# Kernel tuning notes

Measured on AMD Instinct MI355X. Metric: run time of the kernel, lower is better.

The kernel has to match this reference:

```python
import jax, jax.numpy as jnp
import numpy as np

B, N, S, D, K = 8, 8192, 2048, 256, 3
MLP = [256, 128]
EPS = 1e-5


def setup_inputs() -> dict:
    key = jax.random.key(0)
    ks = jax.random.split(key, 12)
    inp = {
        "xyz1": jax.random.normal(ks[0], (B, N, 3), dtype=jnp.float32),
        "xyz2": jax.random.normal(ks[1], (B, S, 3), dtype=jnp.float32),
        "points1": jax.random.normal(ks[2], (B, N, D), dtype=jnp.float32),
        "points2": jax.random.normal(ks[3], (B, S, D), dtype=jnp.float32),
        # relation conv: Conv2d(4 -> 1, kernel 1x1) == linear over last dim
        "rel_w": jax.random.normal(ks[4], (4,), dtype=jnp.float32) * 0.5,
        "rel_b": jnp.zeros((), dtype=jnp.float32),
        # mlp layer 0: Conv1d(2D -> 256, k=1) + BN
        "W0": jax.random.normal(ks[5], (MLP[0], 2 * D), dtype=jnp.float32) * (1.0 / np.sqrt(2 * D)),
        "b0": jnp.zeros((MLP[0],), dtype=jnp.float32),
        "g0": jnp.ones((MLP[0],), dtype=jnp.float32),
        "be0": jnp.zeros((MLP[0],), dtype=jnp.float32),
        # mlp layer 1: Conv1d(256 -> 128, k=1) + BN
        "W1": jax.random.normal(ks[6], (MLP[1], MLP[0]), dtype=jnp.float32) * (1.0 / np.sqrt(MLP[0])),
        "b1": jnp.zeros((MLP[1],), dtype=jnp.float32),
        "g1": jnp.ones((MLP[1],), dtype=jnp.float32),
        "be1": jnp.zeros((MLP[1],), dtype=jnp.float32),
    }
    return inp


def _gather(points, idx):
    # points: [B,S,C], idx: [B,N,K] -> [B,N,K,C]
    return jax.vmap(lambda p, i: p[i])(points, idx)


def _bn_relu(x, gamma, beta):
    # training-mode BatchNorm1d over [B,N,C]: stats over (B,N), biased var
    mean = jnp.mean(x, axis=(0, 1))
    var = jnp.var(x, axis=(0, 1))
    xn = (x - mean) * jax.lax.rsqrt(var + EPS)
    return jax.nn.relu(xn * gamma + beta)


def reference(xyz1, xyz2, points1, points2, rel_w, rel_b,
              W0, b0, g0, be0, W1, b1, g1, be1):
    # pairwise squared distances [B,N,S]
    d = (jnp.sum(xyz1 ** 2, -1)[:, :, None]
         + jnp.sum(xyz2 ** 2, -1)[:, None, :]
         - 2.0 * jnp.einsum('bnc,bmc->bnm', xyz1, xyz2))
    neg_d, idx = jax.lax.top_k(-d, K)          # K smallest distances
    dists = -neg_d                              # [B,N,K]

    offset = xyz1[:, :, None, :] - _gather(xyz2, idx)        # [B,N,K,3]
    rel = jnp.concatenate([dists[..., None], offset], -1)    # [B,N,K,4]
    weight = jax.nn.sigmoid(rel @ rel_w + rel_b)              # [B,N,K]

    interp = jnp.mean(_gather(points2, idx) * weight[..., None], axis=2)  # [B,N,D]
    h = jnp.concatenate([points1, interp], axis=-1)           # [B,N,2D]

    h = _bn_relu(jnp.einsum('bnc,oc->bno', h, W0) + b0, g0, be0)
    h = _bn_relu(jnp.einsum('bnc,oc->bno', h, W1) + b1, g1, be1)
    return h  # [B,N,128]
```

## Files before the change

kernel.cpp:

```cpp
#include <hip/hip_runtime.h>
#include <stdint.h>
#include <stddef.h>

#define B_   8
#define N_   8192
#define S_   2048
#define D_   256
#define M_   (B_*N_)
#define C0_  256
#define C1_  128
#define K2D_ 512
#define TS8_ 8
#define SEG8_ (S_/TS8_)
#define SWP_ 264

typedef __attribute__((ext_vector_type(8))) short short8;
typedef __attribute__((ext_vector_type(4))) float f32x4;
typedef __attribute__((ext_vector_type(2))) float f32x2;

__device__ __forceinline__ short f2bf(float f) {
  unsigned u = __float_as_uint(f);
  u += 0x7fffu + ((u >> 16) & 1u);
  return (short)(u >> 16);
}
__device__ __forceinline__ float bf2f(short s) {
  return __uint_as_float(((unsigned)(unsigned short)s) << 16);
}

__device__ __forceinline__ void cp16(const void* g, void* l) {
  __builtin_amdgcn_global_load_lds(
      (__attribute__((address_space(1))) void*)(g),
      (__attribute__((address_space(3))) void*)(l), 16, 0, 0);
}

#define INS3(v, si)                                                           \
  {                                                                           \
    const float v_ = (v); const int s_ = (si);                                \
    const bool b0 = v_ < d0, b1 = v_ < d1, b2 = v_ < d2;                      \
    const int   ni2 = b1 ? i1 : (b2 ? s_ : i2);                               \
    const float nd2 = __builtin_amdgcn_fmed3f(v_, d1, d2);                    \
    const int   ni1 = b0 ? i0 : (b1 ? s_ : i1);                               \
    const float nd1 = __builtin_amdgcn_fmed3f(v_, d0, d1);                    \
    const int   ni0 = b0 ? s_ : i0;                                           \
    const float nd0 = fminf(v_, d0);                                          \
    d0 = nd0; d1 = nd1; d2 = nd2; i0 = ni0; i1 = ni1; i2 = ni2;               \
  }

__global__ void convw_kernel(const float* __restrict__ W0,
                             const float* __restrict__ W1,
                             const float* __restrict__ xyz2,
                             short* __restrict__ W0b, short* __restrict__ W1b,
                             float* __restrict__ xyz2p, float* __restrict__ stats) {
  int i = blockIdx.x * 256 + threadIdx.x;
  if (blockIdx.x == 0) {
    stats[threadIdx.x] = 0.f;
    stats[256 + threadIdx.x] = 0.f;
    stats[512 + threadIdx.x] = 0.f;
  }
  if (i < C0_ * K2D_) W0b[i] = f2bf(W0[i]);
  if (i < C1_ * C0_)  W1b[i] = f2bf(W1[i]);
  if (i < B_ * S_) {
    const int b = i >> 11, s = i & (S_ - 1);
    float x = xyz2[(size_t)i * 3 + 0];
    float y = xyz2[(size_t)i * 3 + 1];
    float z = xyz2[(size_t)i * 3 + 2];
    float ss = __fadd_rn(__fadd_rn(__fmul_rn(x, x), __fmul_rn(y, y)), __fmul_rn(z, z));
    float* xw = xyz2p + (size_t)b * 4 * S_;
    xw[s] = x; xw[S_ + s] = y; xw[2 * S_ + s] = z; xw[3 * S_ + s] = ss;
  }
}

__global__ __launch_bounds__(512, 8)
void topk_interp_kernel(const float* __restrict__ xyz1, const float* __restrict__ xyz2p,
                        const float* __restrict__ relw, const float* __restrict__ relb,
                        const float* __restrict__ p2, short* __restrict__ hi) {
  __shared__ float cd[TS8_][64][3];
  __shared__ int   ci[TS8_][64][3];
  __shared__ int   sj[64][3];
  __shared__ float sw[64][3];
  const int tid  = threadIdx.x;
  const int lane = tid & 63;
  const int seg  = __builtin_amdgcn_readfirstlane(tid >> 6);
  const int b    = blockIdx.x >> 7;
  const int n    = (blockIdx.x & 127) * 64 + lane;

  const float* p = xyz1 + ((size_t)b * N_ + n) * 3;
  const float ax = p[0], ay = p[1], az = p[2];
  const float s1 = __fadd_rn(__fadd_rn(__fmul_rn(ax, ax), __fmul_rn(ay, ay)), __fmul_rn(az, az));

  const float* xw = xyz2p + (size_t)b * 4 * S_;
  const f32x2* XP = (const f32x2*)(xw)           + seg * (SEG8_ / 2);
  const f32x2* YP = (const f32x2*)(xw + S_)      + seg * (SEG8_ / 2);
  const f32x2* ZP = (const f32x2*)(xw + 2 * S_)  + seg * (SEG8_ / 2);
  const f32x2* WP = (const f32x2*)(xw + 3 * S_)  + seg * (SEG8_ / 2);

  float d0 = 3.4e38f, d1 = 3.4e38f, d2 = 3.4e38f;
  int   i0 = 0, i1 = 0, i2 = 0;
  const int sbeg = seg * SEG8_;
  {
    #pragma clang fp contract(off)
    #pragma unroll 4
    for (int pr = 0; pr < SEG8_ / 2; pr++) {
      f32x2 X = XP[pr], Y = YP[pr], Z = ZP[pr], W = WP[pr];
      f32x2 t1 = ax * X;
      f32x2 t2 = ay * Y;
      f32x2 t3 = az * Z;
      f32x2 dt = (t1 + t2) + t3;
      f32x2 e  = s1 + W;
      f32x2 m  = 2.0f * dt;
      f32x2 d  = e - m;
      const float dlo = d.x, dhi = d.y;
      const int s = sbeg + 2 * pr;
      INS3(dlo, s);
      INS3(dhi, s + 1);
    }
  }
  cd[seg][lane][0] = d0; cd[seg][lane][1] = d1; cd[seg][lane][2] = d2;
  ci[seg][lane][0] = i0; ci[seg][lane][1] = i1; ci[seg][lane][2] = i2;
  __syncthreads();

  if (tid < 64) {
    float d0 = 3.4e38f, d1 = 3.4e38f, d2 = 3.4e38f;
    int   i0 = 0, i1 = 0, i2 = 0;
    #pragma unroll
    for (int sg = 0; sg < TS8_; sg++) {
      #pragma unroll
      for (int k = 0; k < 3; k++) {
        const float dv = cd[sg][tid][k];
        const int   iv = ci[sg][tid][k];
        INS3(dv, iv);
      }
    }
    const float w0r = relw[0], w1r = relw[1], w2r = relw[2], w3r = relw[3], br = relb[0];
    float dd[3] = {d0, d1, d2};
    int   ii[3] = {i0, i1, i2};
    #pragma unroll
    for (int k = 0; k < 3; k++) {
      const int s = ii[k];
      float ox = ax - xw[s], oy = ay - xw[S_ + s], oz = az - xw[2 * S_ + s];
      float t = dd[k] * w0r + ox * w1r + oy * w2r + oz * w3r + br;
      float w = 1.0f / (1.0f + expf(-t));
      sj[tid][k] = s;
      sw[tid][k] = w * (1.0f / 3.0f);
    }
  }
  __syncthreads();

  {
    const int r = tid >> 3;
    const int c0 = (tid & 7) * 32;
    const size_t rowg = (size_t)b * N_ + (size_t)(blockIdx.x & 127) * 64 + r;
    const int j0 = sj[r][0], j1 = sj[r][1], j2 = sj[r][2];
    const float w0 = sw[r][0], w1 = sw[r][1], w2 = sw[r][2];
    const float* pb = p2 + (size_t)b * S_ * D_ + c0;
    const float* q0 = pb + (size_t)j0 * D_;
    const float* q1 = pb + (size_t)j1 * D_;
    const float* q2 = pb + (size_t)j2 * D_;
    short* dst = hi + rowg * D_ + c0;
    #pragma unroll
    for (int cc = 0; cc < 32; cc += 8) {
      const float4 a0 = *(const float4*)(q0 + cc), e0 = *(const float4*)(q0 + cc + 4);
      const float4 a1 = *(const float4*)(q1 + cc), e1 = *(const float4*)(q1 + cc + 4);
      const float4 a2 = *(const float4*)(q2 + cc), e2 = *(const float4*)(q2 + cc + 4);
      float fv[8];
      fv[0] = w0 * a0.x + w1 * a1.x + w2 * a2.x;
      fv[1] = w0 * a0.y + w1 * a1.y + w2 * a2.y;
      fv[2] = w0 * a0.z + w1 * a1.z + w2 * a2.z;
      fv[3] = w0 * a0.w + w1 * a1.w + w2 * a2.w;
      fv[4] = w0 * e0.x + w1 * e1.x + w2 * e2.x;
      fv[5] = w0 * e0.y + w1 * e1.y + w2 * e2.y;
      fv[6] = w0 * e0.z + w1 * e1.z + w2 * e2.z;
      fv[7] = w0 * e0.w + w1 * e1.w + w2 * e2.w;
      short8 o;
      #pragma unroll
      for (int e = 0; e < 8; e++) o[e] = f2bf(fv[e]);
      *(short8*)(dst + cc) = o;
    }
  }
}

__global__ __launch_bounds__(256, 2)
void gemm1_kernel(const float* __restrict__ p1, const short* __restrict__ hi,
                  const short* __restrict__ Bw, const float* __restrict__ bias,
                  short* __restrict__ Cb, float* __restrict__ stats) {
  __shared__ __align__(16) short sA[2][128 * 32];
  __shared__ __align__(16) short sB[2][256 * 32];
  const int tid = threadIdx.x;
  const int lane = tid & 63;
  const int wave = tid >> 6;
  const int wm = wave & 1;
  const int wn = wave >> 1;
  const size_t mbase = (size_t)(blockIdx.x & 7) * N_
                     + (size_t)(blockIdx.x >> 3) * 128;

  #define STAGE_A(K0, BUF)                                                    \
    if ((K0) < D_) {                                                          \
      _Pragma("unroll")                                                       \
      for (int t = 0; t < 2; t++) {                                           \
        const int c = tid * 2 + t;                                            \
        const int r = c >> 2; const int sc = (c & 3) * 8;                     \
        const float* src = p1 + (mbase + r) * D_ + (K0) + sc;                 \
        const float4 va = *(const float4*)src;                                \
        const float4 vb = *(const float4*)(src + 4);                          \
        short8 o;                                                             \
        o[0] = f2bf(va.x); o[1] = f2bf(va.y); o[2] = f2bf(va.z);              \
        o[3] = f2bf(va.w); o[4] = f2bf(vb.x); o[5] = f2bf(vb.y);              \
        o[6] = f2bf(vb.z); o[7] = f2bf(vb.w);                                 \
        *(short8*)&sA[BUF][r * 32 + sc] = o;                                  \
      }                                                                       \
    } else {                                                                  \
      _Pragma("unroll")                                                       \
      for (int t = 0; t < 2; t++) {                                           \
        const int ca = wave * 128 + t * 64 + lane;                            \
        cp16(hi + (mbase + (ca >> 2)) * D_ + ((K0) - D_) + (ca & 3) * 8,      \
             &sA[BUF][(wave * 128 + t * 64) * 8]);                            \
      }                                                                       \
    }

  #define STAGE_B(K0, BUF)                                                    \
    _Pragma("unroll")                                                         \
    for (int t = 0; t < 4; t++) {                                             \
      const int cb = wave * 256 + t * 64 + lane;                              \
      cp16(Bw + (size_t)(cb >> 2) * K2D_ + (K0) + (cb & 3) * 8,               \
           &sB[BUF][(wave * 256 + t * 64) * 8]);                              \
    }

  f32x4 acc[4][8] = {};
  STAGE_A(0, 0);
  STAGE_B(0, 0);

  const int mr = lane & 15;
  const int ks = (lane >> 4) * 8;

  for (int k0 = 0, it = 0; k0 < K2D_; k0 += 32, it++) {
    __syncthreads();
    const int kn = k0 + 32;
    if (kn < K2D_) {
      STAGE_A(kn, (it + 1) & 1);
      STAGE_B(kn, (it + 1) & 1);
    }

    short8 af[4], bfr[8];
    #pragma unroll
    for (int i = 0; i < 4; i++)
      af[i]  = *(const short8*)&sA[it & 1][(wm * 64 + i * 16 + mr) * 32 + ks];
    #pragma unroll
    for (int j = 0; j < 8; j++)
      bfr[j] = *(const short8*)&sB[it & 1][(wn * 128 + j * 16 + mr) * 32 + ks];
    #pragma unroll
    for (int i = 0; i < 4; i++)
      #pragma unroll
      for (int j = 0; j < 8; j++)
        acc[i][j] = __builtin_amdgcn_mfma_f32_16x16x32_bf16(af[i], bfr[j], acc[i][j], 0, 0, 0);
  }
  #undef STAGE_A
  #undef STAGE_B
  __syncthreads();

  const int cr = (lane >> 4) * 4;
  const int cc = lane & 15;
  float ps[8], ps2[8];
  #pragma unroll
  for (int j = 0; j < 8; j++) {
    const int col = wn * 128 + j * 16 + cc;
    const float bv = bias[col];
    float s = 0.f, s2 = 0.f;
    #pragma unroll
    for (int i = 0; i < 4; i++) {
      #pragma unroll
      for (int r = 0; r < 4; r++) {
        const float vv = acc[i][j][r];
        s += vv; s2 += vv * vv;
        const size_t row = mbase + wm * 64 + i * 16 + cr + r;
        Cb[row * C0_ + col] = f2bf(vv + bv);
      }
    }
    ps[j] = s; ps2[j] = s2;
  }
  #pragma unroll
  for (int j = 0; j < 8; j++) {
    ps[j]  += __shfl_xor(ps[j], 16);  ps[j]  += __shfl_xor(ps[j], 32);
    ps2[j] += __shfl_xor(ps2[j], 16); ps2[j] += __shfl_xor(ps2[j], 32);
  }
  float* sred = (float*)sA;
  if (wm == 1 && lane < 16) {
    #pragma unroll
    for (int j = 0; j < 8; j++) {
      const int c = wn * 128 + j * 16 + lane;
      sred[2 * c] = ps[j]; sred[2 * c + 1] = ps2[j];
    }
  }
  __syncthreads();
  if (wm == 0 && lane < 16) {
    #pragma unroll
    for (int j = 0; j < 8; j++) {
      const int c = wn * 128 + j * 16 + lane;
      atomicAdd(&stats[c],       ps[j]  + sred[2 * c]);
      atomicAdd(&stats[C0_ + c], ps2[j] + sred[2 * c + 1]);
    }
  }
}

__global__ __launch_bounds__(256, 2)
void gemm2_kernel(const short* __restrict__ A, const short* __restrict__ Bw,
                  const float* __restrict__ ssn, const float* __restrict__ bias,
                  short* __restrict__ Cb, float* __restrict__ stats) {
  __shared__ __align__(16) short sW[C1_ * SWP_];
  __shared__ float sred[3 * 256];
  const int tid = threadIdx.x;
  const int lane = tid & 63;
  const int wave = tid >> 6;
  const size_t mbase = (size_t)blockIdx.x * 128;

  #pragma unroll
  for (int i = 0; i < 16; i++) {
    const int flat = i * 256 + tid;
    const int n = flat >> 5;
    const int kb = flat & 31;
    *(short8*)&sW[n * SWP_ + kb * 8] = *(const short8*)(Bw + (size_t)flat * 8);
  }
  __syncthreads();

  f32x4 acc[2][8] = {};
  const int mr = lane & 15;
  const int ksq = (lane >> 4) * 8;

  for (int k0 = 0; k0 < C0_; k0 += 32) {
    const int kk = k0 + ksq;
    float4 sc0 = *(const float4*)(ssn + kk);
    float4 sc1 = *(const float4*)(ssn + kk + 4);
    float4 sh0 = *(const float4*)(ssn + C0_ + kk);
    float4 sh1 = *(const float4*)(ssn + C0_ + kk + 4);
    const float sc[8] = {sc0.x, sc0.y, sc0.z, sc0.w, sc1.x, sc1.y, sc1.z, sc1.w};
    const float sh[8] = {sh0.x, sh0.y, sh0.z, sh0.w, sh1.x, sh1.y, sh1.z, sh1.w};
    short8 af[2];
    #pragma unroll
    for (int i = 0; i < 2; i++) {
      const size_t row = mbase + wave * 32 + i * 16 + mr;
      short8 av = *(const short8*)(A + row * C0_ + kk);
      short8 o;
      #pragma unroll
      for (int e = 0; e < 8; e++) {
        float f = bf2f(av[e]) * sc[e] + sh[e];
        o[e] = f2bf(f > 0.f ? f : 0.f);
      }
      af[i] = o;
    }
    short8 bf8[8];
    #pragma unroll
    for (int j = 0; j < 8; j++) bf8[j] = *(const short8*)&sW[(j * 16 + mr) * SWP_ + kk];
    #pragma unroll
    for (int i = 0; i < 2; i++)
      #pragma unroll
      for (int j = 0; j < 8; j++)
        acc[i][j] = __builtin_amdgcn_mfma_f32_16x16x32_bf16(af[i], bf8[j], acc[i][j], 0, 0, 0);
  }

  const int cr = (lane >> 4) * 4;
  const int cc = lane & 15;
  float ps[8], ps2[8];
  #pragma unroll
  for (int j = 0; j < 8; j++) {
    const int col = j * 16 + cc;
    const float bv = bias[col];
    float s = 0.f, s2 = 0.f;
    #pragma unroll
    for (int i = 0; i < 2; i++) {
      #pragma unroll
      for (int r = 0; r < 4; r++) {
        const float vv = acc[i][j][r];
        s += vv; s2 += vv * vv;
        const size_t row = mbase + wave * 32 + i * 16 + cr + r;
        Cb[row * C1_ + col] = f2bf(vv + bv);
      }
    }
    ps[j] = s; ps2[j] = s2;
  }
  #pragma unroll
  for (int j = 0; j < 8; j++) {
    ps[j]  += __shfl_xor(ps[j], 16);  ps[j]  += __shfl_xor(ps[j], 32);
    ps2[j] += __shfl_xor(ps2[j], 16); ps2[j] += __shfl_xor(ps2[j], 32);
  }
  if (wave > 0 && lane < 16) {
    #pragma unroll
    for (int j = 0; j < 8; j++) {
      const int c = j * 16 + lane;
      sred[(wave - 1) * 256 + c]       = ps[j];
      sred[(wave - 1) * 256 + 128 + c] = ps2[j];
    }
  }
  __syncthreads();
  if (wave == 0 && lane < 16) {
    #pragma unroll
    for (int j = 0; j < 8; j++) {
      const int c = j * 16 + lane;
      float s  = ps[j]  + sred[c]       + sred[256 + c]       + sred[512 + c];
      float s2 = ps2[j] + sred[128 + c] + sred[256 + 128 + c] + sred[512 + 128 + c];
      atomicAdd(&stats[c],       s);
      atomicAdd(&stats[C1_ + c], s2);
    }
  }
}

__global__ void stats_final_kernel(const float* __restrict__ stats, const int C,
                                   const float* __restrict__ bias,
                                   const float* __restrict__ g, const float* __restrict__ be,
                                   float* __restrict__ ss) {
  const int c = threadIdx.x;
  if (c >= C) return;
  const float inv = 1.0f / (float)M_;
  float m0 = stats[c] * inv;
  float var = stats[C + c] * inv - m0 * m0;
  float mean = m0 + bias[c];
  float sc = g[c] * rsqrtf(var + 1e-5f);
  ss[c] = sc;
  ss[C + c] = be[c] - mean * sc;
}

__global__ __launch_bounds__(256, 1)
void norm2_kernel(const short* __restrict__ a2, const float* __restrict__ ss,
                  float* __restrict__ out) {
  const size_t t = (size_t)blockIdx.x * 256 + threadIdx.x;
  const size_t base = t * 8;
  const int c = (int)(base & (C1_ - 1));
  short8 v8 = *(const short8*)(a2 + base);
  float vv[8];
  #pragma unroll
  for (int k = 0; k < 8; k++) {
    float v = bf2f(v8[k]) * ss[c + k] + ss[C1_ + c + k];
    vv[k] = v > 0.f ? v : 0.f;
  }
  *(float4*)(out + base)     = make_float4(vv[0], vv[1], vv[2], vv[3]);
  *(float4*)(out + base + 4) = make_float4(vv[4], vv[5], vv[6], vv[7]);
}

extern "C" void kernel_launch(void* const* d_in, const int* in_sizes, int n_in,
                              void* d_out, int out_size, void* d_ws, size_t ws_size,
                              hipStream_t stream) {
  const float* xyz1 = (const float*)d_in[0];
  const float* xyz2 = (const float*)d_in[1];
  const float* pts1 = (const float*)d_in[2];
  const float* pts2 = (const float*)d_in[3];
  const float* relw = (const float*)d_in[4];
  const float* relb = (const float*)d_in[5];
  const float* W0   = (const float*)d_in[6];
  const float* b0   = (const float*)d_in[7];
  const float* g0   = (const float*)d_in[8];
  const float* be0  = (const float*)d_in[9];
  const float* W1   = (const float*)d_in[10];
  const float* b1   = (const float*)d_in[11];
  const float* g1   = (const float*)d_in[12];
  const float* be1  = (const float*)d_in[13];

  char* ws = (char*)d_ws;
  constexpr size_t W0B_OFF = 0;
  constexpr size_t W1B_OFF = W0B_OFF + (size_t)C0_ * K2D_ * 2;
  constexpr size_t XW_OFF  = W1B_OFF + (size_t)C1_ * C0_ * 2;
  constexpr size_t HI_OFF  = XW_OFF + (size_t)B_ * 4 * S_ * 4;
  constexpr size_t A1_OFF  = HI_OFF + (size_t)M_ * D_ * 2;
  constexpr size_t A2_OFF  = A1_OFF + (size_t)M_ * C0_ * 2;
  constexpr size_t ST_OFF  = A2_OFF + (size_t)M_ * C1_ * 2;
  constexpr size_t SS1_OFF = ST_OFF + (size_t)768 * 4;
  constexpr size_t SS2_OFF = SS1_OFF + (size_t)2 * C0_ * 4;

  short* W0b   = (short*)(ws + W0B_OFF);
  short* W1b   = (short*)(ws + W1B_OFF);
  float* xyz2p = (float*)(ws + XW_OFF);
  short* hi    = (short*)(ws + HI_OFF);
  short* a1    = (short*)(ws + A1_OFF);
  short* a2    = (short*)(ws + A2_OFF);
  float* st    = (float*)(ws + ST_OFF);
  float* ss1   = (float*)(ws + SS1_OFF);
  float* ss2   = (float*)(ws + SS2_OFF);
  float* outp  = (float*)d_out;

  convw_kernel<<<512, 256, 0, stream>>>(W0, W1, xyz2, W0b, W1b, xyz2p, st);
  topk_interp_kernel<<<B_ * (N_ / 64), 512, 0, stream>>>(xyz1, xyz2p, relw, relb, pts2, hi);

  gemm1_kernel<<<M_ / 128, 256, 0, stream>>>(pts1, hi, W0b, b0, a1, st);
  stats_final_kernel<<<1, 256, 0, stream>>>(st, C0_, b0, g0, be0, ss1);

  gemm2_kernel<<<M_ / 128, 256, 0, stream>>>(a1, W1b, ss1, b1, a2, st + 512);
  stats_final_kernel<<<1, 128, 0, stream>>>(st + 512, C1_, b1, g1, be1, ss2);
  norm2_kernel<<<(size_t)M_ * C1_ / 8 / 256, 256, 0, stream>>>(a2, ss2, outp);
}
```

Measured before the change: 282.8 us.

## Pack distance and index into doubles for top-3, fold BN finalize into consumers

The top-3 nearest search now packs each clamped non-negative float distance and its index into the low mantissa bits of a double. The sorted insert then uses only fmin/fmax on doubles instead of compare-and-select on separate float and int registers. The two stats_final launches are removed: gemm2 and norm2 each compute the BN scale and shift from the raw sums in shared memory, which saves two tiny kernel launches. FP64 min/max may run at a different rate than FP32 on this hardware, and the per-block redundant finalize adds a small amount of work to every block.

```diff
diff --git a/kernel.cpp b/kernel.cpp
--- a/kernel.cpp
+++ b/kernel.cpp
@@ -33,17 +33,17 @@
       (__attribute__((address_space(3))) void*)(l), 16, 0, 0);
 }
 
-#define INS3(v, si)                                                           \
+__device__ __forceinline__ double packdi(float d, int s) {
+  return __longlong_as_double(__double_as_longlong((double)d) |
+                              (unsigned long long)(unsigned)s);
+}
+
+#define PINS(v)                                                               \
   {                                                                           \
-    const float v_ = (v); const int s_ = (si);                                \
-    const bool b0 = v_ < d0, b1 = v_ < d1, b2 = v_ < d2;                      \
-    const int   ni2 = b1 ? i1 : (b2 ? s_ : i2);                               \
-    const float nd2 = __builtin_amdgcn_fmed3f(v_, d1, d2);                    \
-    const int   ni1 = b0 ? i0 : (b1 ? s_ : i1);                               \
-    const float nd1 = __builtin_amdgcn_fmed3f(v_, d0, d1);                    \
-    const int   ni0 = b0 ? s_ : i0;                                           \
-    const float nd0 = fminf(v_, d0);                                          \
-    d0 = nd0; d1 = nd1; d2 = nd2; i0 = ni0; i1 = ni1; i2 = ni2;               \
+    const double v_ = (v);                                                    \
+    double t_ = fmax(a0, v_); a0 = fmin(a0, v_);                              \
+    double u_ = fmax(a1, t_); a1 = fmin(a1, t_);                              \
+    a2 = fmin(a2, u_);                                                        \
   }
 
 __global__ void convw_kernel(const float* __restrict__ W0,
@@ -74,8 +74,7 @@
 void topk_interp_kernel(const float* __restrict__ xyz1, const float* __restrict__ xyz2p,
                         const float* __restrict__ relw, const float* __restrict__ relb,
                         const float* __restrict__ p2, short* __restrict__ hi) {
-  __shared__ float cd[TS8_][64][3];
-  __shared__ int   ci[TS8_][64][3];
+  __shared__ double cdp[TS8_][64][3];
   __shared__ int   sj[64][3];
   __shared__ float sw[64][3];
   const int tid  = threadIdx.x;
@@ -94,8 +93,7 @@
   const f32x2* ZP = (const f32x2*)(xw + 2 * S_)  + seg * (SEG8_ / 2);
   const f32x2* WP = (const f32x2*)(xw + 3 * S_)  + seg * (SEG8_ / 2);
 
-  float d0 = 3.4e38f, d1 = 3.4e38f, d2 = 3.4e38f;
-  int   i0 = 0, i1 = 0, i2 = 0;
+  double a0 = 1e300, a1 = 1e300, a2 = 1e300;
   const int sbeg = seg * SEG8_;
   {
     #pragma clang fp contract(off)
@@ -109,36 +107,35 @@
       f32x2 e  = s1 + W;
       f32x2 m  = 2.0f * dt;
       f32x2 d  = e - m;
-      const float dlo = d.x, dhi = d.y;
+      const float dlo = fmaxf(d.x, 0.f), dhi = fmaxf(d.y, 0.f);
       const int s = sbeg + 2 * pr;
-      INS3(dlo, s);
-      INS3(dhi, s + 1);
-    }
-  }
-  cd[seg][lane][0] = d0; cd[seg][lane][1] = d1; cd[seg][lane][2] = d2;
-  ci[seg][lane][0] = i0; ci[seg][lane][1] = i1; ci[seg][lane][2] = i2;
+      const double p0 = packdi(dlo, s);
+      const double p1 = packdi(dhi, s + 1);
+      PINS(p0);
+      PINS(p1);
+    }
+  }
+  cdp[seg][lane][0] = a0; cdp[seg][lane][1] = a1; cdp[seg][lane][2] = a2;
   __syncthreads();
 
   if (tid < 64) {
-    float d0 = 3.4e38f, d1 = 3.4e38f, d2 = 3.4e38f;
-    int   i0 = 0, i1 = 0, i2 = 0;
+    double a0 = 1e300, a1 = 1e300, a2 = 1e300;
     #pragma unroll
     for (int sg = 0; sg < TS8_; sg++) {
       #pragma unroll
       for (int k = 0; k < 3; k++) {
-        const float dv = cd[sg][tid][k];
-        const int   iv = ci[sg][tid][k];
-        INS3(dv, iv);
+        const double v = cdp[sg][tid][k];
+        PINS(v);
       }
     }
     const float w0r = relw[0], w1r = relw[1], w2r = relw[2], w3r = relw[3], br = relb[0];
-    float dd[3] = {d0, d1, d2};
-    int   ii[3] = {i0, i1, i2};
+    const double pk[3] = {a0, a1, a2};
     #pragma unroll
     for (int k = 0; k < 3; k++) {
-      const int s = ii[k];
+      const int s = (int)(__double_as_longlong(pk[k]) & 2047ULL);
+      const float dk = (float)pk[k];
       float ox = ax - xw[s], oy = ay - xw[S_ + s], oz = az - xw[2 * S_ + s];
-      float t = dd[k] * w0r + ox * w1r + oy * w2r + oz * w3r + br;
+      float t = dk * w0r + ox * w1r + oy * w2r + oz * w3r + br;
       float w = 1.0f / (1.0f + expf(-t));
       sj[tid][k] = s;
       sw[tid][k] = w * (1.0f / 3.0f);
@@ -159,14 +156,14 @@
     short* dst = hi + rowg * D_ + c0;
     #pragma unroll
     for (int cc = 0; cc < 32; cc += 8) {
-      const float4 a0 = *(const float4*)(q0 + cc), e0 = *(const float4*)(q0 + cc + 4);
-      const float4 a1 = *(const float4*)(q1 + cc), e1 = *(const float4*)(q1 + cc + 4);
-      const float4 a2 = *(const float4*)(q2 + cc), e2 = *(const float4*)(q2 + cc + 4);
+      const float4 a0v = *(const float4*)(q0 + cc), e0 = *(const float4*)(q0 + cc + 4);
+      const float4 a1v = *(const float4*)(q1 + cc), e1 = *(const float4*)(q1 + cc + 4);
+      const float4 a2v = *(const float4*)(q2 + cc), e2 = *(const float4*)(q2 + cc + 4);
       float fv[8];
-      fv[0] = w0 * a0.x + w1 * a1.x + w2 * a2.x;
-      fv[1] = w0 * a0.y + w1 * a1.y + w2 * a2.y;
-      fv[2] = w0 * a0.z + w1 * a1.z + w2 * a2.z;
-      fv[3] = w0 * a0.w + w1 * a1.w + w2 * a2.w;
+      fv[0] = w0 * a0v.x + w1 * a1v.x + w2 * a2v.x;
+      fv[1] = w0 * a0v.y + w1 * a1v.y + w2 * a2v.y;
+      fv[2] = w0 * a0v.z + w1 * a1v.z + w2 * a2v.z;
+      fv[3] = w0 * a0v.w + w1 * a1v.w + w2 * a2v.w;
       fv[4] = w0 * e0.x + w1 * e1.x + w2 * e2.x;
       fv[5] = w0 * e0.y + w1 * e1.y + w2 * e2.y;
       fv[6] = w0 * e0.z + w1 * e1.z + w2 * e2.z;
@@ -303,14 +300,28 @@
 
 __global__ __launch_bounds__(256, 2)
 void gemm2_kernel(const short* __restrict__ A, const short* __restrict__ Bw,
-                  const float* __restrict__ ssn, const float* __restrict__ bias,
+                  const float* __restrict__ st1,
+                  const float* __restrict__ b0, const float* __restrict__ g0,
+                  const float* __restrict__ be0,
+                  const float* __restrict__ bias,
                   short* __restrict__ Cb, float* __restrict__ stats) {
   __shared__ __align__(16) short sW[C1_ * SWP_];
   __shared__ float sred[3 * 256];
+  __shared__ __align__(16) float sss[2 * C0_];
   const int tid = threadIdx.x;
   const int lane = tid & 63;
   const int wave = tid >> 6;
   const size_t mbase = (size_t)blockIdx.x * 128;
+
+  {
+    const float inv = 1.0f / (float)M_;
+    const float m0 = st1[tid] * inv;
+    const float var = st1[C0_ + tid] * inv - m0 * m0;
+    const float mean = m0 + b0[tid];
+    const float sc = g0[tid] * rsqrtf(var + 1e-5f);
+    sss[tid] = sc;
+    sss[C0_ + tid] = be0[tid] - mean * sc;
+  }
 
   #pragma unroll
   for (int i = 0; i < 16; i++) {
@@ -327,10 +338,10 @@
 
   for (int k0 = 0; k0 < C0_; k0 += 32) {
     const int kk = k0 + ksq;
-    float4 sc0 = *(const float4*)(ssn + kk);
-    float4 sc1 = *(const float4*)(ssn + kk + 4);
-    float4 sh0 = *(const float4*)(ssn + C0_ + kk);
-    float4 sh1 = *(const float4*)(ssn + C0_ + kk + 4);
+    float4 sc0 = *(const float4*)&sss[kk];
+    float4 sc1 = *(const float4*)&sss[kk + 4];
+    float4 sh0 = *(const float4*)&sss[C0_ + kk];
+    float4 sh1 = *(const float4*)&sss[C0_ + kk + 4];
     const float sc[8] = {sc0.x, sc0.y, sc0.z, sc0.w, sc1.x, sc1.y, sc1.z, sc1.w};
     const float sh[8] = {sh0.x, sh0.y, sh0.z, sh0.w, sh1.x, sh1.y, sh1.z, sh1.w};
     short8 af[2];
@@ -402,32 +413,30 @@
   }
 }
 
-__global__ void stats_final_kernel(const float* __restrict__ stats, const int C,
-                                   const float* __restrict__ bias,
-                                   const float* __restrict__ g, const float* __restrict__ be,
-                                   float* __restrict__ ss) {
-  const int c = threadIdx.x;
-  if (c >= C) return;
-  const float inv = 1.0f / (float)M_;
-  float m0 = stats[c] * inv;
-  float var = stats[C + c] * inv - m0 * m0;
-  float mean = m0 + bias[c];
-  float sc = g[c] * rsqrtf(var + 1e-5f);
-  ss[c] = sc;
-  ss[C + c] = be[c] - mean * sc;
-}
-
 __global__ __launch_bounds__(256, 1)
-void norm2_kernel(const short* __restrict__ a2, const float* __restrict__ ss,
-                  float* __restrict__ out) {
-  const size_t t = (size_t)blockIdx.x * 256 + threadIdx.x;
+void norm2_kernel(const short* __restrict__ a2, const float* __restrict__ st2,
+                  const float* __restrict__ b1, const float* __restrict__ g1,
+                  const float* __restrict__ be1, float* __restrict__ out) {
+  __shared__ __align__(16) float sss[2 * C1_];
+  const int tid = threadIdx.x;
+  if (tid < C1_) {
+    const float inv = 1.0f / (float)M_;
+    const float m0 = st2[tid] * inv;
+    const float var = st2[C1_ + tid] * inv - m0 * m0;
+    const float mean = m0 + b1[tid];
+    const float sc = g1[tid] * rsqrtf(var + 1e-5f);
+    sss[tid] = sc;
+    sss[C1_ + tid] = be1[tid] - mean * sc;
+  }
+  __syncthreads();
+  const size_t t = (size_t)blockIdx.x * 256 + tid;
   const size_t base = t * 8;
   const int c = (int)(base & (C1_ - 1));
   short8 v8 = *(const short8*)(a2 + base);
   float vv[8];
   #pragma unroll
   for (int k = 0; k < 8; k++) {
-    float v = bf2f(v8[k]) * ss[c + k] + ss[C1_ + c + k];
+    float v = bf2f(v8[k]) * sss[c + k] + sss[C1_ + c + k];
     vv[k] = v > 0.f ? v : 0.f;
   }
   *(float4*)(out + base)     = make_float4(vv[0], vv[1], vv[2], vv[3]);
@@ -460,8 +469,6 @@
   constexpr size_t A1_OFF  = HI_OFF + (size_t)M_ * D_ * 2;
   constexpr size_t A2_OFF  = A1_OFF + (size_t)M_ * C0_ * 2;
   constexpr size_t ST_OFF  = A2_OFF + (size_t)M_ * C1_ * 2;
-  constexpr size_t SS1_OFF = ST_OFF + (size_t)768 * 4;
-  constexpr size_t SS2_OFF = SS1_OFF + (size_t)2 * C0_ * 4;
 
   short* W0b   = (short*)(ws + W0B_OFF);
   short* W1b   = (short*)(ws + W1B_OFF);
@@ -470,17 +477,12 @@
   short* a1    = (short*)(ws + A1_OFF);
   short* a2    = (short*)(ws + A2_OFF);
   float* st    = (float*)(ws + ST_OFF);
-  float* ss1   = (float*)(ws + SS1_OFF);
-  float* ss2   = (float*)(ws + SS2_OFF);
   float* outp  = (float*)d_out;
 
   convw_kernel<<<512, 256, 0, stream>>>(W0, W1, xyz2, W0b, W1b, xyz2p, st);
   topk_interp_kernel<<<B_ * (N_ / 64), 512, 0, stream>>>(xyz1, xyz2p, relw, relb, pts2, hi);
 
   gemm1_kernel<<<M_ / 128, 256, 0, stream>>>(pts1, hi, W0b, b0, a1, st);
-  stats_final_kernel<<<1, 256, 0, stream>>>(st, C0_, b0, g0, be0, ss1);
-
-  gemm2_kernel<<<M_ / 128, 256, 0, stream>>>(a1, W1b, ss1, b1, a2, st + 512);
-  stats_final_kernel<<<1, 128, 0, stream>>>(st + 512, C1_, b1, g1, be1, ss2);
-  norm2_kernel<<<(size_t)M_ * C1_ / 8 / 256, 256, 0, stream>>>(a2, ss2, outp);
-}
+  gemm2_kernel<<<M_ / 128, 256, 0, stream>>>(a1, W1b, st, b0, g0, be0, b1, a2, st + 512);
+  norm2_kernel<<<(size_t)M_ * C1_ / 8 / 256, 256, 0, stream>>>(a2, st + 512, b1, g1, be1, outp);
+}
```

Measured after the change: 277.7 us. No clear change (-1.8%).
